# Performance work log

Measured on AMD Instinct MI355X. Metric: run time of the kernel, lower is better.

The kernel has to match this reference:

```python
import jax, jax.numpy as jnp
import numpy as np

NEG_SLOPE = 0.2


def setup_inputs() -> dict:
    key = jax.random.key(0)
    ks = jax.random.split(key, 10)
    V, E, Din, Dout, H = 50000, 800000, 128, 128, 4
    h = jax.random.normal(ks[0], (V, Din), dtype=jnp.float32)
    edge_index = jax.random.randint(ks[1], (2, E), 0, V, dtype=jnp.int32)
    edge_weight = jax.random.uniform(ks[2], (E,), dtype=jnp.float32)
    s = 1.0 / np.sqrt(Din)
    Wq = jax.random.normal(ks[3], (Din, Dout), dtype=jnp.float32) * s
    Wk = jax.random.normal(ks[4], (Din, Dout), dtype=jnp.float32) * s
    Wv = jax.random.normal(ks[5], (Din, Dout), dtype=jnp.float32) * s
    Wo = jax.random.normal(ks[6], (Dout, Dout), dtype=jnp.float32) * (1.0 / np.sqrt(Dout))
    We = jax.random.normal(ks[7], (1, H), dtype=jnp.float32)
    bq = jnp.zeros((Dout,), jnp.float32)
    bk = jnp.zeros((Dout,), jnp.float32)
    bv = jnp.zeros((Dout,), jnp.float32)
    bo = jnp.zeros((Dout,), jnp.float32)
    be = jnp.zeros((H,), jnp.float32)
    return {"h": h, "edge_index": edge_index, "edge_weight": edge_weight,
            "Wq": Wq, "bq": bq, "Wk": Wk, "bk": bk, "Wv": Wv, "bv": bv,
            "Wo": Wo, "bo": bo, "We": We, "be": be}


def reference(h, edge_index, edge_weight, Wq, bq, Wk, bk, Wv, bv, Wo, bo, We, be):
    V = h.shape[0]
    H = be.shape[0]
    Dout = Wq.shape[1]
    F_h = Dout // H

    # Node projections -> [V, H, F_h]
    Q = (h @ Wq + bq).reshape(V, H, F_h)
    K = (h @ Wk + bk).reshape(V, H, F_h)
    Vv = (h @ Wv + bv).reshape(V, H, F_h)

    # Edge bias: Linear(1, H) on edge_weight, then LeakyReLU -> [E, H]
    edge_bias = jax.nn.leaky_relu(edge_weight[:, None] @ We + be, negative_slope=NEG_SLOPE)

    src, tgt = edge_index[0], edge_index[1]

    # Per-edge attention logits: dot(Q[src], K[tgt]) / sqrt(F_h) + bias -> [E, H]
    attn_raw = jnp.sum(Q[src] * K[tgt], axis=-1) / jnp.sqrt(jnp.float32(F_h)) + edge_bias
    attn_exp = jnp.exp(attn_raw)  # faithful: original uses unshifted exp

    # Scatter-softmax normalizer per target node -> [V, H]
    deg = jax.ops.segment_sum(attn_exp, tgt, num_segments=V) + 1e-16
    attn_norm = attn_exp / deg[tgt]  # [E, H]

    # Weighted messages and scatter-sum to targets
    msg = Vv[src] * attn_norm[:, :, None] * edge_weight[:, None, None]  # [E, H, F_h]
    out = jax.ops.segment_sum(msg, tgt, num_segments=V)  # [V, H, F_h]

    out = out.reshape(V, H * F_h)
    out = jax.nn.leaky_relu(out @ Wo + bo, negative_slope=NEG_SLOPE)
    return out
```

## Files before the change

kernel.cpp:

```cpp
#include <hip/hip_runtime.h>
#include <hip/hip_bf16.h>

#define NEG_SLOPE 0.2f

typedef __attribute__((ext_vector_type(8))) short bf16x8;
typedef __attribute__((ext_vector_type(4))) float f32x4;

__device__ __forceinline__ void splitf(float x, unsigned short& h, unsigned short& l)
{
    const unsigned int u  = __float_as_uint(x);
    const unsigned int uh = (u + 0x7fffu + ((u >> 16) & 1u)) >> 16;
    const float        fh = __uint_as_float(uh << 16);
    const float        r  = x - fh;
    const unsigned int ur = __float_as_uint(r);
    const unsigned int ul = (ur + 0x7fffu + ((ur >> 16) & 1u)) >> 16;
    h = (unsigned short)uh;
    l = (unsigned short)ul;
}

__global__ __launch_bounds__(256) void prep(
    const float* __restrict__ Wq, const float* __restrict__ Wk,
    const float* __restrict__ Wv, const float* __restrict__ Wo,
    unsigned short* __restrict__ Wth, unsigned short* __restrict__ Wtl,
    const int* __restrict__ tgt, int* __restrict__ cnt, int E)
{
    const int bid = blockIdx.x;
    if (bid < 256) {
        const int mat = bid >> 6;
        const float* __restrict__ W =
            (mat == 0) ? Wq : ((mat == 1) ? Wk : ((mat == 2) ? Wv : Wo));
        const int t = (bid & 63) * 256 + threadIdx.x;
        const int k = t >> 7, n = t & 127;
        unsigned short h, l;
        splitf(W[k * 128 + n], h, l);
        Wth[mat * 16384 + n * 128 + k] = h;
        Wtl[mat * 16384 + n * 128 + k] = l;
    } else {
        const int e = (bid - 256) * 256 + threadIdx.x;
        if (e < E) atomicAdd(cnt + tgt[e], 1);
    }
}

__global__ __launch_bounds__(256) void scan1(const int* __restrict__ cnt,
                                             int* __restrict__ offs,
                                             int* __restrict__ bsums, int V)
{
    __shared__ int sh[256];
    const int t = threadIdx.x;
    const int base = blockIdx.x * 1024;
    int v[4];
    int s = 0;
#pragma unroll
    for (int i = 0; i < 4; ++i) {
        const int idx = base + t * 4 + i;
        v[i] = (idx < V) ? cnt[idx] : 0;
        s += v[i];
    }
    sh[t] = s;
    __syncthreads();
    for (int off = 1; off < 256; off <<= 1) {
        const int x = (t >= off) ? sh[t - off] : 0;
        __syncthreads();
        sh[t] += x;
        __syncthreads();
    }
    int run = (t > 0) ? sh[t - 1] : 0;
#pragma unroll
    for (int i = 0; i < 4; ++i) {
        const int idx = base + t * 4 + i;
        if (idx < V) offs[idx] = run;
        run += v[i];
    }
    if (t == 255) bsums[blockIdx.x] = sh[255];
}

__global__ void scan2(int* __restrict__ bsums, int nb)
{
    if (threadIdx.x == 0 && blockIdx.x == 0) {
        int run = 0;
        for (int i = 0; i < nb; ++i) { const int x = bsums[i]; bsums[i] = run; run += x; }
    }
}

__global__ __launch_bounds__(256) void scan3(int* __restrict__ offs,
                                             const int* __restrict__ bsums,
                                             int* __restrict__ fill, int V)
{
    const int v = blockIdx.x * blockDim.x + threadIdx.x;
    if (v >= V) return;
    const int o = offs[v] + bsums[v >> 10];
    offs[v] = o;
    fill[v] = o;
}

__global__ __launch_bounds__(256) void scatter_edges(
    const int* __restrict__ src, const int* __restrict__ tgt,
    const float* __restrict__ ew, int* __restrict__ fill,
    int2* __restrict__ se, int E)
{
    const int e = blockIdx.x * blockDim.x + threadIdx.x;
    if (e >= E) return;
    const int pos = atomicAdd(fill + tgt[e], 1);
    se[pos] = make_int2(src[e], __float_as_int(ew[e]));
}

__global__ __launch_bounds__(256) void gemm_mfma(
    const float* __restrict__ A,
    const unsigned short* __restrict__ Bh0, const unsigned short* __restrict__ Bl0,
    const unsigned short* __restrict__ Bh1, const unsigned short* __restrict__ Bl1,
    const unsigned short* __restrict__ Bh2, const unsigned short* __restrict__ Bl2,
    const float* __restrict__ b0, const float* __restrict__ b1, const float* __restrict__ b2,
    float* __restrict__ D0, float* __restrict__ D1, float* __restrict__ D2,
    int V, int lrelu)
{
    __shared__ unsigned short Ash[64][40], Asl[64][40];
    __shared__ unsigned short Bsh[128][40], Bsl[128][40];

    const int m = blockIdx.y;
    const unsigned short* __restrict__ Wth = (m == 0) ? Bh0 : ((m == 1) ? Bh1 : Bh2);
    const unsigned short* __restrict__ Wtl = (m == 0) ? Bl0 : ((m == 1) ? Bl1 : Bl2);
    const float* __restrict__ bias         = (m == 0) ? b0  : ((m == 1) ? b1  : b2);
    float* __restrict__ D                  = (m == 0) ? D0  : ((m == 1) ? D1  : D2);

    const int tid  = threadIdx.x;
    const int w    = tid >> 6;
    const int l    = tid & 63;
    const int row0 = blockIdx.x * 64;

    const int srow = tid >> 2;
    const int skc  = tid & 3;

    f32x4 acc[8];
#pragma unroll
    for (int t = 0; t < 8; ++t) acc[t] = (f32x4){0.f, 0.f, 0.f, 0.f};

    for (int k0 = 0; k0 < 128; k0 += 32) {
        {
            const int gr = row0 + srow;
            float x[8] = {0.f, 0.f, 0.f, 0.f, 0.f, 0.f, 0.f, 0.f};
            if (gr < V) {
                const float4 a0 = *(const float4*)(A + (size_t)gr * 128 + k0 + skc * 8);
                const float4 a1 = *(const float4*)(A + (size_t)gr * 128 + k0 + skc * 8 + 4);
                x[0] = a0.x; x[1] = a0.y; x[2] = a0.z; x[3] = a0.w;
                x[4] = a1.x; x[5] = a1.y; x[6] = a1.z; x[7] = a1.w;
            }
            bf16x8 vh, vl;
#pragma unroll
            for (int i = 0; i < 8; ++i) {
                unsigned short hh, ll;
                splitf(x[i], hh, ll);
                vh[i] = (short)hh; vl[i] = (short)ll;
            }
            *(bf16x8*)&Ash[srow][skc * 8] = vh;
            *(bf16x8*)&Asl[srow][skc * 8] = vl;
        }
#pragma unroll
        for (int r = 0; r < 2; ++r) {
            const int idx = tid + r * 256;
            const int n = idx >> 2, bkc = idx & 3;
            *(bf16x8*)&Bsh[n][bkc * 8] = *(const bf16x8*)(Wth + n * 128 + k0 + bkc * 8);
            *(bf16x8*)&Bsl[n][bkc * 8] = *(const bf16x8*)(Wtl + n * 128 + k0 + bkc * 8);
        }
        __syncthreads();

        const int ar  = w * 16 + (l & 15);
        const int kc8 = (l >> 4) * 8;
        const bf16x8 ah = *(const bf16x8*)&Ash[ar][kc8];
        const bf16x8 al = *(const bf16x8*)&Asl[ar][kc8];
#pragma unroll
        for (int t = 0; t < 8; ++t) {
            const int col = t * 16 + (l & 15);
            const bf16x8 bh = *(const bf16x8*)&Bsh[col][kc8];
            const bf16x8 bl = *(const bf16x8*)&Bsl[col][kc8];
            acc[t] = __builtin_amdgcn_mfma_f32_16x16x32_bf16(ah, bh, acc[t], 0, 0, 0);
            acc[t] = __builtin_amdgcn_mfma_f32_16x16x32_bf16(ah, bl, acc[t], 0, 0, 0);
            acc[t] = __builtin_amdgcn_mfma_f32_16x16x32_bf16(al, bh, acc[t], 0, 0, 0);
        }
        __syncthreads();
    }

    const int colb = l & 15;
    const int rsub = (l >> 4) * 4;
#pragma unroll
    for (int t = 0; t < 8; ++t) {
        const int col = t * 16 + colb;
        const float bv = bias[col];
#pragma unroll
        for (int r = 0; r < 4; ++r) {
            const int grow = row0 + w * 16 + rsub + r;
            if (grow < V) {
                float xx = acc[t][r] + bv;
                if (lrelu) xx = (xx > 0.f) ? xx : NEG_SLOPE * xx;
                D[(size_t)grow * 128 + col] = xx;
            }
        }
    }
}

__global__ __launch_bounds__(256) void fused_agg(
    const float* __restrict__ Q, const float* __restrict__ K,
    const float* __restrict__ Vv, const int2* __restrict__ se,
    const int* __restrict__ offs, const int* __restrict__ fill,
    const float* __restrict__ Wei, const float* __restrict__ bei,
    float* __restrict__ accum, int V)
{
    __shared__ float Ksh[4][4][36];
    const int wid = threadIdx.x >> 6;
    const int node = blockIdx.x * 4 + wid;
    if (node >= V) return;
    const int l   = threadIdx.x & 63;
    const int h   = l & 3;
    const int hd  = l >> 4;
    const float weH = Wei[h], beH = bei[h];
    const float2* __restrict__ Vv2 = (const float2*)Vv;

    {
        const float2 kk = *(const float2*)(K + (size_t)node * 128 + l * 2);
        const int f0 = l * 2;
        Ksh[wid][f0 >> 5][f0 & 31] = kk.x;
        Ksh[wid][(f0 + 1) >> 5][(f0 + 1) & 31] = kk.y;
    }

    const int start = offs[node];
    const int end   = fill[node];

    float degacc = 0.f;
    float ax = 0.f, ay = 0.f;

    for (int b0 = start; b0 < end; b0 += 16) {
        const int nj = min(16, end - b0);
        const int jj = l >> 2;
        int   s = 0;
        float w = 0.f, p = 0.f;
        if (jj < nj) {
            const int2 t = se[b0 + jj];
            s = t.x;
            w = __int_as_float(t.y);
            const float4* qp = (const float4*)(Q + (size_t)s * 128 + h * 32);
            float dot = 0.f;
#pragma unroll
            for (int i = 0; i < 8; ++i) {
                const float4 q = qp[i];
                const float4 k = *(const float4*)&Ksh[wid][h][i * 4];
                dot += q.x * k.x + q.y * k.y + q.z * k.z + q.w * k.w;
            }
            float bb = fmaf(w, weH, beH);
            bb = (bb > 0.f) ? bb : NEG_SLOPE * bb;
            p = __expf(fmaf(dot, 0.17677669529663687f, bb));
        }
        degacc += p;
        const float coef = p * w;

        if (nj == 16) {
#pragma unroll
            for (int j = 0; j < 16; ++j) {
                const float cj = __shfl(coef, j * 4 + hd);
                const int   sj = __shfl(s,    j * 4);
                const float2 v = Vv2[(size_t)sj * 64 + l];
                ax = fmaf(cj, v.x, ax);
                ay = fmaf(cj, v.y, ay);
            }
        } else {
            for (int j = 0; j < nj; ++j) {
                const float cj = __shfl(coef, j * 4 + hd);
                const int   sj = __shfl(s,    j * 4);
                const float2 v = Vv2[(size_t)sj * 64 + l];
                ax = fmaf(cj, v.x, ax);
                ay = fmaf(cj, v.y, ay);
            }
        }
    }

    float d = degacc;
    d += __shfl_xor(d, 4);
    d += __shfl_xor(d, 8);
    d += __shfl_xor(d, 16);
    d += __shfl_xor(d, 32);
    const float deg = __shfl(d, hd);
    const float inv = 1.0f / (deg + 1e-16f);

    *(float2*)(accum + (size_t)node * 128 + l * 2) =
        make_float2(ax * inv, ay * inv);
}

extern "C" void kernel_launch(void* const* d_in, const int* in_sizes, int n_in,
                              void* d_out, int out_size, void* d_ws, size_t ws_size,
                              hipStream_t stream)
{
    const float* h   = (const float*)d_in[0];
    const int*   ei  = (const int*)  d_in[1];
    const float* ew  = (const float*)d_in[2];
    const float* Wq  = (const float*)d_in[3];
    const float* bq  = (const float*)d_in[4];
    const float* Wk  = (const float*)d_in[5];
    const float* bk  = (const float*)d_in[6];
    const float* Wv  = (const float*)d_in[7];
    const float* bv  = (const float*)d_in[8];
    const float* Wo  = (const float*)d_in[9];
    const float* bo  = (const float*)d_in[10];
    const float* Wei = (const float*)d_in[11];
    const float* bei = (const float*)d_in[12];

    const int V = in_sizes[0] / 128;
    const int E = in_sizes[2];
    const int* src = ei;
    const int* tgt = ei + E;

    float* Q     = (float*)d_ws;
    float* Km    = Q  + (size_t)V * 128;
    float* Vm    = Km + (size_t)V * 128;
    float* accum = Vm + (size_t)V * 128;
    unsigned short* Wth = (unsigned short*)(accum + (size_t)V * 128);
    unsigned short* Wtl = Wth + 4 * 16384;
    int2*  se    = (int2*)(Wtl + 4 * 16384);
    int*   cnt   = (int*)(se + E);
    int*   offs  = cnt  + V;
    int*   fill  = offs + V + 1;
    int*   bsums = fill + V;

    hipMemsetAsync(cnt, 0, (size_t)V * sizeof(int), stream);

    prep<<<256 + (E + 255) / 256, 256, 0, stream>>>(
        Wq, Wk, Wv, Wo, Wth, Wtl, tgt, cnt, E);

    const int mfGrid = (V + 63) / 64;
    gemm_mfma<<<dim3(mfGrid, 3), 256, 0, stream>>>(
        h, Wth, Wtl, Wth + 16384, Wtl + 16384, Wth + 2 * 16384, Wtl + 2 * 16384,
        bq, bk, bv, Q, Km, Vm, V, 0);

    const int nb = (V + 1023) / 1024;
    scan1<<<nb, 256, 0, stream>>>(cnt, offs, bsums, V);
    scan2<<<1, 64, 0, stream>>>(bsums, nb);
    scan3<<<(V + 255) / 256, 256, 0, stream>>>(offs, bsums, fill, V);
    scatter_edges<<<(E + 255) / 256, 256, 0, stream>>>(
        src, tgt, ew, fill, se, E);

    fused_agg<<<(V + 3) / 4, 256, 0, stream>>>(
        Q, Km, Vm, se, offs, fill, Wei, bei, accum, V);

    gemm_mfma<<<dim3(mfGrid, 1), 256, 0, stream>>>(
        accum, Wth + 3 * 16384, Wtl + 3 * 16384, Wth + 3 * 16384, Wtl + 3 * 16384,
        Wth + 3 * 16384, Wtl + 3 * 16384,
        bo, bo, bo, (float*)d_out, (float*)d_out, (float*)d_out, V, 1);
}
```

Measured before the change: 277.5 us.

## Interleave Q and V rows and fold block-sum scan into scan3

Stores Q and V projections interleaved per node (256-float rows) so the gathered source row for both the attention dot and the message lives in one contiguous 1KB region, improving locality in the edge aggregation. The GEMM gains per-output leading dimensions to write into the interleaved buffer. It also removes the single-thread scan2 launch by having each scan3 block sum the preceding block totals itself, trading a launch for a small redundant serial loop per block.

```diff
diff --git a/kernel.cpp b/kernel.cpp
--- a/kernel.cpp
+++ b/kernel.cpp
@@ -74,21 +74,21 @@
     if (t == 255) bsums[blockIdx.x] = sh[255];
 }
 
-__global__ void scan2(int* __restrict__ bsums, int nb)
-{
-    if (threadIdx.x == 0 && blockIdx.x == 0) {
-        int run = 0;
-        for (int i = 0; i < nb; ++i) { const int x = bsums[i]; bsums[i] = run; run += x; }
-    }
-}
-
 __global__ __launch_bounds__(256) void scan3(int* __restrict__ offs,
                                              const int* __restrict__ bsums,
                                              int* __restrict__ fill, int V)
 {
+    __shared__ int pref;
     const int v = blockIdx.x * blockDim.x + threadIdx.x;
+    const int chunk = (blockIdx.x * blockDim.x) >> 10;
+    if (threadIdx.x == 0) {
+        int s = 0;
+        for (int i = 0; i < chunk; ++i) s += bsums[i];
+        pref = s;
+    }
+    __syncthreads();
     if (v >= V) return;
-    const int o = offs[v] + bsums[v >> 10];
+    const int o = offs[v] + pref;
     offs[v] = o;
     fill[v] = o;
 }
@@ -111,6 +111,7 @@
     const unsigned short* __restrict__ Bh2, const unsigned short* __restrict__ Bl2,
     const float* __restrict__ b0, const float* __restrict__ b1, const float* __restrict__ b2,
     float* __restrict__ D0, float* __restrict__ D1, float* __restrict__ D2,
+    int ld0, int ld1, int ld2,
     int V, int lrelu)
 {
     __shared__ unsigned short Ash[64][40], Asl[64][40];
@@ -121,6 +122,7 @@
     const unsigned short* __restrict__ Wtl = (m == 0) ? Bl0 : ((m == 1) ? Bl1 : Bl2);
     const float* __restrict__ bias         = (m == 0) ? b0  : ((m == 1) ? b1  : b2);
     float* __restrict__ D                  = (m == 0) ? D0  : ((m == 1) ? D1  : D2);
+    const int ldD                          = (m == 0) ? ld0 : ((m == 1) ? ld1 : ld2);
 
     const int tid  = threadIdx.x;
     const int w    = tid >> 6;
@@ -191,15 +193,15 @@
             if (grow < V) {
                 float xx = acc[t][r] + bv;
                 if (lrelu) xx = (xx > 0.f) ? xx : NEG_SLOPE * xx;
-                D[(size_t)grow * 128 + col] = xx;
+                D[(size_t)grow * ldD + col] = xx;
             }
         }
     }
 }
 
 __global__ __launch_bounds__(256) void fused_agg(
-    const float* __restrict__ Q, const float* __restrict__ K,
-    const float* __restrict__ Vv, const int2* __restrict__ se,
+    const float* __restrict__ QV, const float* __restrict__ K,
+    const int2* __restrict__ se,
     const int* __restrict__ offs, const int* __restrict__ fill,
     const float* __restrict__ Wei, const float* __restrict__ bei,
     float* __restrict__ accum, int V)
@@ -212,7 +214,7 @@
     const int h   = l & 3;
     const int hd  = l >> 4;
     const float weH = Wei[h], beH = bei[h];
-    const float2* __restrict__ Vv2 = (const float2*)Vv;
+    const float2* __restrict__ Vv2 = (const float2*)(QV + 128);
 
     {
         const float2 kk = *(const float2*)(K + (size_t)node * 128 + l * 2);
@@ -236,7 +238,7 @@
             const int2 t = se[b0 + jj];
             s = t.x;
             w = __int_as_float(t.y);
-            const float4* qp = (const float4*)(Q + (size_t)s * 128 + h * 32);
+            const float4* qp = (const float4*)(QV + (size_t)s * 256 + h * 32);
             float dot = 0.f;
 #pragma unroll
             for (int i = 0; i < 8; ++i) {
@@ -256,7 +258,7 @@
             for (int j = 0; j < 16; ++j) {
                 const float cj = __shfl(coef, j * 4 + hd);
                 const int   sj = __shfl(s,    j * 4);
-                const float2 v = Vv2[(size_t)sj * 64 + l];
+                const float2 v = Vv2[(size_t)sj * 128 + l];
                 ax = fmaf(cj, v.x, ax);
                 ay = fmaf(cj, v.y, ay);
             }
@@ -264,7 +266,7 @@
             for (int j = 0; j < nj; ++j) {
                 const float cj = __shfl(coef, j * 4 + hd);
                 const int   sj = __shfl(s,    j * 4);
-                const float2 v = Vv2[(size_t)sj * 64 + l];
+                const float2 v = Vv2[(size_t)sj * 128 + l];
                 ax = fmaf(cj, v.x, ax);
                 ay = fmaf(cj, v.y, ay);
             }
@@ -306,10 +308,9 @@
     const int* src = ei;
     const int* tgt = ei + E;
 
-    float* Q     = (float*)d_ws;
-    float* Km    = Q  + (size_t)V * 128;
-    float* Vm    = Km + (size_t)V * 128;
-    float* accum = Vm + (size_t)V * 128;
+    float* QV    = (float*)d_ws;
+    float* Km    = QV + (size_t)V * 256;
+    float* accum = Km + (size_t)V * 128;
     unsigned short* Wth = (unsigned short*)(accum + (size_t)V * 128);
     unsigned short* Wtl = Wth + 4 * 16384;
     int2*  se    = (int2*)(Wtl + 4 * 16384);
@@ -326,20 +327,20 @@
     const int mfGrid = (V + 63) / 64;
     gemm_mfma<<<dim3(mfGrid, 3), 256, 0, stream>>>(
         h, Wth, Wtl, Wth + 16384, Wtl + 16384, Wth + 2 * 16384, Wtl + 2 * 16384,
-        bq, bk, bv, Q, Km, Vm, V, 0);
+        bq, bk, bv, QV, Km, QV + 128, 256, 128, 256, V, 0);
 
     const int nb = (V + 1023) / 1024;
     scan1<<<nb, 256, 0, stream>>>(cnt, offs, bsums, V);
-    scan2<<<1, 64, 0, stream>>>(bsums, nb);
     scan3<<<(V + 255) / 256, 256, 0, stream>>>(offs, bsums, fill, V);
     scatter_edges<<<(E + 255) / 256, 256, 0, stream>>>(
         src, tgt, ew, fill, se, E);
 
     fused_agg<<<(V + 3) / 4, 256, 0, stream>>>(
-        Q, Km, Vm, se, offs, fill, Wei, bei, accum, V);
+        QV, Km, se, offs, fill, Wei, bei, accum, V);
 
     gemm_mfma<<<dim3(mfGrid, 1), 256, 0, stream>>>(
         accum, Wth + 3 * 16384, Wtl + 3 * 16384, Wth + 3 * 16384, Wtl + 3 * 16384,
         Wth + 3 * 16384, Wtl + 3 * 16384,
-        bo, bo, bo, (float*)d_out, (float*)d_out, (float*)d_out, V, 1);
-}
+        bo, bo, bo, (float*)d_out, (float*)d_out, (float*)d_out,
+        128, 128, 128, V, 1);
+}
```

Result: no change. 273.1 us (-1.6%).
